# Kernel tuning notes

Hardware: AMD Instinct MI355X
Metric: run time of the kernel (lower is better)

The kernel has to match this reference:

```python
import jax, jax.numpy as jnp
import numpy as np

B, S, DIM, HDIM = 8, 1024, 1024, 128
H = DIM // HDIM  # 8 heads
GN_EPS = 1e-3    # keras GroupNormalization default epsilon


def group_norm(y, gamma, beta, groups, eps=GN_EPS):
    # keras GroupNormalization on [B,S,C]: reshape to [B,S,groups,C//groups],
    # normalize over all axes except batch and group axis -> axes (1,3).
    b, s, c = y.shape
    g = y.reshape(b, s, groups, c // groups)
    mean = g.mean(axis=(1, 3), keepdims=True)
    var = g.var(axis=(1, 3), keepdims=True)
    g = (g - mean) * jax.lax.rsqrt(var + eps)
    return g.reshape(b, s, c) * gamma + beta


def setup_inputs() -> dict:
    key = jax.random.key(0)
    ks = jax.random.split(key, 7)
    x = jax.random.normal(ks[0], (B, S, DIM), dtype=jnp.float32)
    sc_h = 1.0 / np.sqrt(HDIM).astype(np.float32)
    sc_d = 1.0 / np.sqrt(DIM).astype(np.float32)
    Wq = jax.random.normal(ks[1], (H, HDIM, HDIM), dtype=jnp.float32) * sc_h
    Wk = jax.random.normal(ks[2], (H, HDIM, HDIM), dtype=jnp.float32) * sc_h
    Wv = jax.random.normal(ks[3], (H, HDIM, HDIM), dtype=jnp.float32) * sc_h
    Wg = jax.random.normal(ks[4], (DIM, DIM), dtype=jnp.float32) * sc_d
    Wo = jax.random.normal(ks[5], (DIM, DIM), dtype=jnp.float32) * sc_d
    gn_gamma = jnp.ones((DIM,), dtype=jnp.float32)
    gn_beta = jnp.zeros((DIM,), dtype=jnp.float32)
    return {"x": x, "Wq": Wq, "Wk": Wk, "Wv": Wv, "Wg": Wg, "Wo": Wo,
            "gn_gamma": gn_gamma, "gn_beta": gn_beta}


def reference(x, Wq, Wk, Wv, Wg, Wo, gn_gamma, gn_beta):
    b, s, c = x.shape
    h, hd = Wq.shape[0], Wq.shape[1]
    # gating branch: W = ReLU(x @ Wg)
    Wgate = jax.nn.relu(jnp.einsum('bsc,cd->bsd', x, Wg))
    # split channels into heads: [B,S,H,hd]
    xh = x.reshape(b, s, h, hd)
    Q = jnp.einsum('bshd,hde->bhse', xh, Wq)
    K = jnp.einsum('bshd,hde->bhse', xh, Wk)
    V = jnp.einsum('bshd,hde->bhse', xh, Wv)
    # per-head decay mask D[h,i,j] = gamma_h ** (i - j) (full, non-causal as in source)
    idx = jnp.arange(s, dtype=jnp.float32)
    gammas = 1.0 - 2.0 ** (-5.0 - jnp.arange(h, dtype=jnp.float32))  # [H]
    decay = gammas[:, None, None] ** (idx[None, :, None] - idx[None, None, :])  # [H,S,S]
    scores = jnp.einsum('bhsd,bhtd->bhst', Q, K) * decay[None]
    ret = jnp.einsum('bhst,bhtd->bhsd', scores, V)       # [B,H,S,hd]
    y = ret.transpose(0, 2, 1, 3).reshape(b, s, c)        # concat heads
    Y = group_norm(y, gn_gamma, gn_beta, groups=hd)       # groups = hdim (keras arg)
    return jnp.einsum('bsc,cd->bsd', Wgate * Y, Wo)
```

## Files before the change

### kernel.cpp

```cpp
#include <hip/hip_runtime.h>

#define BB 8
#define SS 1024
#define DD 1024
#define HH 8
#define HD 128
#define GN_EPS 1e-3f

typedef __attribute__((ext_vector_type(8))) short bf16x8;
typedef __attribute__((ext_vector_type(4))) float f32x4;

__device__ __forceinline__ short f2bf(float f) {
    unsigned u = __float_as_uint(f);
    return (short)((u + 0x7fffu + ((u >> 16) & 1u)) >> 16);
}
__device__ __forceinline__ float bf2f(short s) {
    return __uint_as_float(((unsigned)(unsigned short)s) << 16);
}

__device__ __forceinline__ void gload16(const void* g, void* l) {
    __builtin_amdgcn_global_load_lds((const __attribute__((address_space(1))) void*)g,
                                     (__attribute__((address_space(3))) void*)l, 16, 0, 0);
}

__device__ __forceinline__ void stage_tile(const short* __restrict__ G, size_t ld, int k0,
                                           short* lds, int wid, int lane) {
#pragma unroll
    for (int i = 0; i < 2; i++) {
        const int seg = wid * 2 + i;
        const int row = seg * 8 + (lane >> 3);
        const int chunk = (lane & 7) ^ (lane >> 3);
        gload16(G + (size_t)row * ld + k0 + chunk * 8, lds + seg * 512);
    }
}

__device__ __forceinline__ void gemm_tile_g(
    const short* __restrict__ A, size_t ldA,
    const short* __restrict__ B, size_t ldB,
    int K, short* As, short* Bs, f32x4 acc[4][2])
{
    const int tid = threadIdx.x, lane = tid & 63, wid = tid >> 6;
    const int wr = (wid >> 2) * 64, wc = (wid & 3) * 32;
    const int fr = lane & 15, fc = lane >> 4;
    const int rsw = fr & 7;
#pragma unroll
    for (int i = 0; i < 4; i++)
#pragma unroll
        for (int j = 0; j < 2; j++) acc[i][j] = (f32x4){0.f, 0.f, 0.f, 0.f};

    const int nt = K >> 6;
    stage_tile(A, ldA, 0, As, wid, lane);
    stage_tile(B, ldB, 0, Bs, wid, lane);
    if (nt > 1) {
        stage_tile(A, ldA, 64, As + 8192, wid, lane);
        stage_tile(B, ldB, 64, Bs + 8192, wid, lane);
    }
    for (int t = 0; t < nt; t++) {
        if (t + 1 < nt) asm volatile("s_waitcnt vmcnt(4)" ::: "memory");
        else            asm volatile("s_waitcnt vmcnt(0)" ::: "memory");
        __builtin_amdgcn_s_barrier();
        __builtin_amdgcn_sched_barrier(0);
        const int cur = t & 1;
        const short* as = As + (cur << 13);
        const short* bs = Bs + (cur << 13);
#pragma unroll
        for (int half = 0; half < 2; half++) {
            const int slot = ((half * 4 + fc) ^ rsw) << 3;
            bf16x8 af[4], bfv[2];
#pragma unroll
            for (int i = 0; i < 4; i++) af[i] = *(const bf16x8*)&as[(wr + i * 16 + fr) * 64 + slot];
#pragma unroll
            for (int j = 0; j < 2; j++) bfv[j] = *(const bf16x8*)&bs[(wc + j * 16 + fr) * 64 + slot];
#pragma unroll
            for (int i = 0; i < 4; i++)
#pragma unroll
                for (int j = 0; j < 2; j++)
                    acc[i][j] = __builtin_amdgcn_mfma_f32_16x16x32_bf16(af[i], bfv[j], acc[i][j], 0, 0, 0);
        }
        __builtin_amdgcn_sched_barrier(0);
        asm volatile("s_waitcnt lgkmcnt(0)" ::: "memory");
        __builtin_amdgcn_s_barrier();
        if (t + 2 < nt) {
            stage_tile(A, ldA, (t + 2) << 6, As + (cur << 13), wid, lane);
            stage_tile(B, ldB, (t + 2) << 6, Bs + (cur << 13), wid, lane);
        }
    }
}

__device__ __forceinline__ void stage_A32(const short* __restrict__ G, size_t ld, int k0,
                                          short* lds, int wid, int lane) {
#pragma unroll
    for (int i = 0; i < 2; i++) {
        const int row = wid * 32 + i * 16 + (lane >> 2);
        const int chunk = (lane & 3) ^ ((row >> 1) & 3);
        gload16(G + (size_t)row * ld + k0 + chunk * 8, lds + wid * 1024 + i * 512);
    }
}
__device__ __forceinline__ void stage_B32(const short* __restrict__ G, size_t ld, int k0,
                                          short* lds, int wid, int lane) {
    const int row = wid * 16 + (lane >> 2);
    const int chunk = (lane & 3) ^ ((row >> 1) & 3);
    gload16(G + (size_t)row * ld + k0 + chunk * 8, lds + wid * 512);
}

__device__ __forceinline__ void gemm_tile_n(
    const short* __restrict__ A, size_t ldA,
    const short* __restrict__ B, size_t ldB,
    int K, short* As, short* Bs, f32x4 acc[4][4])
{
    const int tid = threadIdx.x, lane = tid & 63, wid = tid >> 6;
    const int wr = (wid >> 1) * 64, wc = (wid & 1) * 64;
    const int fr = lane & 15, fc = lane >> 4;
    const int slot = (fc ^ ((fr >> 1) & 3)) << 3;
#pragma unroll
    for (int i = 0; i < 4; i++)
#pragma unroll
        for (int j = 0; j < 4; j++) acc[i][j] = (f32x4){0.f, 0.f, 0.f, 0.f};

    const int nt = K >> 5;
    stage_A32(A, ldA, 0, As, wid, lane);
    stage_B32(B, ldB, 0, Bs, wid, lane);
    if (nt > 1) {
        stage_A32(A, ldA, 32, As + 8192, wid, lane);
        stage_B32(B, ldB, 32, Bs + 4096, wid, lane);
    }
    for (int t = 0; t < nt; t++) {
        if (t + 1 < nt) asm volatile("s_waitcnt vmcnt(3)" ::: "memory");
        else            asm volatile("s_waitcnt vmcnt(0)" ::: "memory");
        __builtin_amdgcn_s_barrier();
        __builtin_amdgcn_sched_barrier(0);
        const int cur = t & 1;
        const short* as = As + (cur << 13);
        const short* bs = Bs + (cur << 12);
        bf16x8 af[4], bfv[4];
#pragma unroll
        for (int i = 0; i < 4; i++) af[i] = *(const bf16x8*)&as[(wr + i * 16 + fr) * 32 + slot];
#pragma unroll
        for (int j = 0; j < 4; j++) bfv[j] = *(const bf16x8*)&bs[(wc + j * 16 + fr) * 32 + slot];
#pragma unroll
        for (int i = 0; i < 4; i++)
#pragma unroll
            for (int j = 0; j < 4; j++)
                acc[i][j] = __builtin_amdgcn_mfma_f32_16x16x32_bf16(af[i], bfv[j], acc[i][j], 0, 0, 0);
        __builtin_amdgcn_sched_barrier(0);
        asm volatile("s_waitcnt lgkmcnt(0)" ::: "memory");
        __builtin_amdgcn_s_barrier();
        if (t + 2 < nt) {
            stage_A32(A, ldA, (t + 2) << 5, As + (cur << 13), wid, lane);
            stage_B32(B, ldB, (t + 2) << 5, Bs + (cur << 12), wid, lane);
        }
    }
}

__global__ __launch_bounds__(256) void prep(
    const float* __restrict__ x,
    const float* __restrict__ Wq, const float* __restrict__ Wk, const float* __restrict__ Wv,
    const float* __restrict__ Wg, const float* __restrict__ Wo,
    short* __restrict__ xb, short* __restrict__ WgT, short* __restrict__ WoT,
    short* __restrict__ Wt, float* __restrict__ sQ, float* __restrict__ sK,
    float* __restrict__ Sp)
{
    __shared__ float t[32][33];
    int bid = blockIdx.x;
    const int tid = threadIdx.x;
    if (bid < 4096) {
        const size_t i = ((size_t)bid * 256 + tid) * 8;
        float4 a = *(const float4*)&x[i];
        float4 b = *(const float4*)&x[i + 4];
        bf16x8 v;
        v[0] = f2bf(a.x); v[1] = f2bf(a.y); v[2] = f2bf(a.z); v[3] = f2bf(a.w);
        v[4] = f2bf(b.x); v[5] = f2bf(b.y); v[6] = f2bf(b.z); v[7] = f2bf(b.w);
        *(bf16x8*)&xb[i] = v;
        return;
    }
    bid -= 4096;
    if (bid < 2048) {
        const float* __restrict__ S = (bid < 1024) ? Wg : Wo;
        short* __restrict__ D = (bid < 1024) ? WgT : WoT;
        const int tb = bid & 1023;
        const int bx = (tb & 31) * 32, by = (tb >> 5) * 32;
        const int xx = tid & 31, y0 = tid >> 5;
#pragma unroll
        for (int r = 0; r < 32; r += 8) t[y0 + r][xx] = S[(size_t)(by + y0 + r) * 1024 + bx + xx];
        __syncthreads();
#pragma unroll
        for (int r = 0; r < 32; r += 8) D[(size_t)(bx + y0 + r) * 1024 + by + xx] = f2bf(t[xx][y0 + r]);
        return;
    }
    bid -= 2048;
    if (bid < 384) {
        const int ht = bid >> 4, tb = bid & 15;
        const int typ = ht >> 3, h = ht & 7;
        const float* __restrict__ W = (typ == 0 ? Wq : (typ == 1 ? Wk : Wv)) + (size_t)h * HD * HD;
        short* __restrict__ D = Wt + (size_t)ht * HD * HD;
        const int bx = (tb & 3) * 32, by = (tb >> 2) * 32;
        const int xx = tid & 31, y0 = tid >> 5;
#pragma unroll
        for (int r = 0; r < 32; r += 8) t[y0 + r][xx] = W[(by + y0 + r) * HD + bx + xx];
        __syncthreads();
#pragma unroll
        for (int r = 0; r < 32; r += 8) D[(bx + y0 + r) * HD + by + xx] = f2bf(t[xx][y0 + r]);
        return;
    }
    bid -= 384;
    if (bid < 32) {
        const int h = bid >> 2;
        const int s = (bid & 3) * 256 + tid;
        const double gamma = 1.0 - exp2((double)(-5 - h));
        const double lg = log2(gamma);
        sQ[h * SS + s] = (float)exp2(lg * (double)s);
        sK[h * SS + s] = (float)exp2(-lg * (double)s);
        return;
    }
    *(float4*)&Sp[tid * 8] = (float4){0.f, 0.f, 0.f, 0.f};
    *(float4*)&Sp[tid * 8 + 4] = (float4){0.f, 0.f, 0.f, 0.f};
}

__global__ __launch_bounds__(512) void g_qkvgate(
    const short* __restrict__ xb, const short* __restrict__ Wt, const short* __restrict__ WgT,
    const float* __restrict__ sQ, const float* __restrict__ sK,
    short* __restrict__ Qb, short* __restrict__ Ktb, short* __restrict__ Vtb,
    short* __restrict__ gateb)
{
    __shared__ short As[2 * 8192], Bs[2 * 8192];
    const int orig = blockIdx.x;
    const int cx = orig & 7, p = orig >> 3;
    const int tid = threadIdx.x, lane = tid & 63, wid = tid >> 6;
    const int r0 = (lane >> 4) * 4, c = lane & 15;

    if (p < 32) {
        f32x4 acc[4][4];
        const int w2 = cx * 32 + p;
        const int m0 = (w2 >> 3) * 256, n0 = (w2 & 7) * 128;
        gemm_tile_n(xb + (size_t)m0 * DD, DD, WgT + (size_t)n0 * DD, DD, DD, As, Bs, acc);
        const int wr = (wid >> 1) * 64, wc = (wid & 1) * 64;
#pragma unroll
        for (int i = 0; i < 4; i++)
#pragma unroll
            for (int j = 0; j < 4; j++)
#pragma unroll
                for (int r = 0; r < 4; r++)
                    gateb[(size_t)(m0 + wr + i * 16 + r0 + r) * DD + n0 + wc + j * 16 + c] =
                        f2bf(fmaxf(acc[i][j][r], 0.f));
        return;
    }
    f32x4 acc[4][2];
    const int w = cx * 64 + (p - 32);
    const int mt = w >> 3, h = w & 7;
    const int m0 = mt * 128;
    const int b = m0 >> 10, s0 = m0 & (SS - 1);
    const int bh = (b << 3) + h;
    const short* __restrict__ A = xb + (size_t)m0 * DD + h * HD;
    const int wr = (wid >> 2) * 64, wc = (wid & 3) * 32;
    const int fr = lane & 15, fc = lane >> 4;
    const int rsw = fr & 7;

    stage_tile(A, DD, 0,  As,        wid, lane);
    stage_tile(A, DD, 64, As + 8192, wid, lane);
    stage_tile(Wt + (size_t)h * HD * HD, HD, 0, Bs, wid, lane);
    __syncthreads();

#pragma unroll
    for (int i = 0; i < 4; i++)
#pragma unroll
        for (int j = 0; j < 2; j++) acc[i][j] = (f32x4){0.f, 0.f, 0.f, 0.f};

    int sb = 0;
    for (int st = 0; st < 6; st++) {
        if (st + 1 < 6) {
            const int typn = (st + 1) >> 1, ktn = (st + 1) & 1;
            stage_tile(Wt + (size_t)(typn * 8 + h) * HD * HD, HD, ktn * 64,
                       Bs + ((sb ^ 1) << 13), wid, lane);
        }
        const int kt = st & 1;
        const short* as = As + (kt << 13);
        const short* bs = Bs + (sb << 13);
#pragma unroll
        for (int half = 0; half < 2; half++) {
            const int slot = ((half * 4 + fc) ^ rsw) << 3;
            bf16x8 af[4], bfv[2];
#pragma unroll
            for (int i = 0; i < 4; i++) af[i] = *(const bf16x8*)&as[(wr + i * 16 + fr) * 64 + slot];
#pragma unroll
            for (int j = 0; j < 2; j++) bfv[j] = *(const bf16x8*)&bs[(wc + j * 16 + fr) * 64 + slot];
#pragma unroll
            for (int i = 0; i < 4; i++)
#pragma unroll
                for (int j = 0; j < 2; j++)
                    acc[i][j] = __builtin_amdgcn_mfma_f32_16x16x32_bf16(af[i], bfv[j], acc[i][j], 0, 0, 0);
        }
        __syncthreads();
        sb ^= 1;
        if (kt == 1) {
            const int typ = st >> 1;
            if (typ == 0) {
#pragma unroll
                for (int i = 0; i < 4; i++)
#pragma unroll
                    for (int j = 0; j < 2; j++)
#pragma unroll
                        for (int r = 0; r < 4; r++) {
                            const int s = s0 + wr + i * 16 + r0 + r;
                            Qb[((size_t)bh * SS + s) * HD + wc + j * 16 + c] =
                                f2bf(acc[i][j][r] * sQ[h * SS + s]);
                        }
            } else if (typ == 1) {
                short* __restrict__ Ob = Ktb + (size_t)bh * HD * SS;
#pragma unroll
                for (int i = 0; i < 4; i++)
#pragma unroll
                    for (int j = 0; j < 2; j++) {
                        const int tb = s0 + wr + i * 16 + r0;
                        const int d = wc + j * 16 + c;
                        short4 o;
                        o.x = f2bf(acc[i][j][0] * sK[h * SS + tb + 0]);
                        o.y = f2bf(acc[i][j][1] * sK[h * SS + tb + 1]);
                        o.z = f2bf(acc[i][j][2] * sK[h * SS + tb + 2]);
                        o.w = f2bf(acc[i][j][3] * sK[h * SS + tb + 3]);
                        *(short4*)&Ob[(size_t)d * SS + tb] = o;
                    }
            } else {
                short* __restrict__ Ob = Vtb + (size_t)bh * HD * SS;
#pragma unroll
                for (int i = 0; i < 4; i++)
#pragma unroll
                    for (int j = 0; j < 2; j++) {
                        const int tb = s0 + wr + i * 16 + r0;
                        const int e = wc + j * 16 + c;
                        short4 o;
                        o.x = f2bf(acc[i][j][0]); o.y = f2bf(acc[i][j][1]);
                        o.z = f2bf(acc[i][j][2]); o.w = f2bf(acc[i][j][3]);
                        *(short4*)&Ob[(size_t)e * SS + tb] = o;
                    }
            }
#pragma unroll
            for (int i = 0; i < 4; i++)
#pragma unroll
                for (int j = 0; j < 2; j++) acc[i][j] = (f32x4){0.f, 0.f, 0.f, 0.f};
        }
    }
}

__global__ __launch_bounds__(512) void g_kv(
    const short* __restrict__ Vtb, const short* __restrict__ Ktb, float* __restrict__ Mp)
{
    __shared__ short As[2 * 8192], Bs[2 * 8192];
    f32x4 acc[4][2];
    const int orig = blockIdx.x;
    const int w = (orig & 7) * 16 + (orig >> 3);
    const int chunk = w & 1, bh = w >> 1;
    gemm_tile_g(Vtb + (size_t)bh * HD * SS + chunk * 512, SS,
                Ktb + (size_t)bh * HD * SS + chunk * 512, SS, 512, As, Bs, acc);
    const int tid = threadIdx.x, lane = tid & 63, wid = tid >> 6;
    const int wr = (wid >> 2) * 64, wc = (wid & 3) * 32;
    const int r0 = (lane >> 4) * 4, c = lane & 15;
    float* __restrict__ Ob = Mp + (size_t)w * HD * HD;
#pragma unroll
    for (int i = 0; i < 4; i++)
#pragma unroll
        for (int j = 0; j < 2; j++)
#pragma unroll
            for (int r = 0; r < 4; r++)
                Ob[(size_t)(wr + i * 16 + r0 + r) * HD + wc + j * 16 + c] = acc[i][j][r];
}

__global__ __launch_bounds__(256) void g_mredcvt(const float* __restrict__ Mp, short* __restrict__ Mtb) {
    const size_t i = ((size_t)blockIdx.x * 256 + threadIdx.x) * 8;
    const size_t bh = i >> 14, ij = i & 16383;
    const float* p = Mp + (bh * 2) * 16384 + ij;
    float s[8];
#pragma unroll
    for (int q = 0; q < 8; q++) s[q] = 0.f;
#pragma unroll
    for (int cth = 0; cth < 2; cth++) {
        float4 a = *(const float4*)&p[cth * 16384];
        float4 b = *(const float4*)&p[cth * 16384 + 4];
        s[0] += a.x; s[1] += a.y; s[2] += a.z; s[3] += a.w;
        s[4] += b.x; s[5] += b.y; s[6] += b.z; s[7] += b.w;
    }
    bf16x8 v;
#pragma unroll
    for (int q = 0; q < 8; q++) v[q] = f2bf(s[q]);
    *(bf16x8*)&Mtb[i] = v;
}

__global__ __launch_bounds__(512) void g_qm(
    const short* __restrict__ Qb, const short* __restrict__ Mtb,
    short* __restrict__ retc, float* __restrict__ Sp)
{
    __shared__ short As[2 * 8192], Bs[2 * 8192];
    f32x4 acc[4][2];
    const int orig = blockIdx.x;
    const int w = (orig & 7) * 64 + (orig >> 3);
    const int bh = w >> 3, m0 = (w & 7) * 128;
    const short* __restrict__ A = Qb + ((size_t)bh * SS + m0) * HD;
    const short* __restrict__ Bp = Mtb + (size_t)bh * HD * HD;
    const int tid = threadIdx.x, lane = tid & 63, wid = tid >> 6;
    const int wr = (wid >> 2) * 64, wc = (wid & 3) * 32;
    const int fr = lane & 15, fc = lane >> 4, rsw = fr & 7;
    const int r0 = (lane >> 4) * 4, c = lane & 15;

    stage_tile(A,  HD, 0,  As,        wid, lane);
    stage_tile(A,  HD, 64, As + 8192, wid, lane);
    stage_tile(Bp, HD, 0,  Bs,        wid, lane);
    stage_tile(Bp, HD, 64, Bs + 8192, wid, lane);
#pragma unroll
    for (int i = 0; i < 4; i++)
#pragma unroll
        for (int j = 0; j < 2; j++) acc[i][j] = (f32x4){0.f, 0.f, 0.f, 0.f};
    asm volatile("s_waitcnt vmcnt(0)" ::: "memory");
    __builtin_amdgcn_s_barrier();
    __builtin_amdgcn_sched_barrier(0);
#pragma unroll
    for (int kt = 0; kt < 2; kt++) {
        const short* as = As + (kt << 13);
        const short* bs = Bs + (kt << 13);
#pragma unroll
        for (int half = 0; half < 2; half++) {
            const int slot = ((half * 4 + fc) ^ rsw) << 3;
            bf16x8 af[4], bfv[2];
#pragma unroll
            for (int i = 0; i < 4; i++) af[i] = *(const bf16x8*)&as[(wr + i * 16 + fr) * 64 + slot];
#pragma unroll
            for (int j = 0; j < 2; j++) bfv[j] = *(const bf16x8*)&bs[(wc + j * 16 + fr) * 64 + slot];
#pragma unroll
            for (int i = 0; i < 4; i++)
#pragma unroll
                for (int j = 0; j < 2; j++)
                    acc[i][j] = __builtin_amdgcn_mfma_f32_16x16x32_bf16(af[i], bfv[j], acc[i][j], 0, 0, 0);
        }
    }
    const int b_ = bh >> 3, h_ = bh & 7;
    short* __restrict__ O = retc + ((size_t)(b_ * SS + m0)) * DD + h_ * HD;
#pragma unroll
    for (int i = 0; i < 4; i++)
#pragma unroll
        for (int j = 0; j < 2; j++)
#pragma unroll
            for (int r = 0; r < 4; r++)
                O[(size_t)(wr + i * 16 + r0 + r) * DD + wc + j * 16 + c] = f2bf(acc[i][j][r]);

    float psm[2], psq[2];
#pragma unroll
    for (int j = 0; j < 2; j++) { psm[j] = 0.f; psq[j] = 0.f; }
#pragma unroll
    for (int i = 0; i < 4; i++)
#pragma unroll
        for (int j = 0; j < 2; j++)
#pragma unroll
            for (int r = 0; r < 4; r++) {
                const float v = acc[i][j][r];
                psm[j] += v; psq[j] += v * v;
            }
    const int masks[5] = {1, 2, 4, 16, 32};
#pragma unroll
    for (int mk = 0; mk < 5; mk++) {
#pragma unroll
        for (int j = 0; j < 2; j++) {
            psm[j] += __shfl_xor(psm[j], masks[mk], 64);
            psq[j] += __shfl_xor(psq[j], masks[mk], 64);
        }
    }
    if ((lane & 7) == 0 && lane < 16) {
        const int hi = lane >> 3;
#pragma unroll
        for (int j = 0; j < 2; j++) {
            const int g = b_ * 128 + h_ * 16 + (wid & 3) * 4 + j * 2 + hi;
            atomicAdd(&Sp[g * 2 + 0], psm[j]);
            atomicAdd(&Sp[g * 2 + 1], psq[j]);
        }
    }
}

__global__ __launch_bounds__(256) void aprep(
    const short* __restrict__ gateb, const short* __restrict__ retc,
    const float* __restrict__ Sp,
    const float* __restrict__ gng, const float* __restrict__ gnb, short* __restrict__ Ab)
{
    const size_t idx = ((size_t)blockIdx.x * 256 + threadIdx.x) * 4;
    const int m = (int)(idx >> 10), cc = (int)(idx & 1023);
    const int b_ = m >> 10, g = b_ * 128 + (cc >> 3);
    const float sm = Sp[g * 2 + 0], sq = Sp[g * 2 + 1];
    const float mu = sm * (1.0f / 8192.0f);
    float var = sq * (1.0f / 8192.0f) - mu * mu;
    if (var < 0.f) var = 0.f;
    const float rs = rsqrtf(var + GN_EPS);
    short4 gv4 = *(const short4*)&gateb[idx];
    short4 rv4 = *(const short4*)&retc[idx];
    float4 gv = *(const float4*)&gng[cc];
    float4 bv = *(const float4*)&gnb[cc];
    short4 o;
    o.x = f2bf(bf2f(gv4.x) * ((bf2f(rv4.x) - mu) * rs * gv.x + bv.x));
    o.y = f2bf(bf2f(gv4.y) * ((bf2f(rv4.y) - mu) * rs * gv.y + bv.y));
    o.z = f2bf(bf2f(gv4.z) * ((bf2f(rv4.z) - mu) * rs * gv.z + bv.z));
    o.w = f2bf(bf2f(gv4.w) * ((bf2f(rv4.w) - mu) * rs * gv.w + bv.w));
    *(short4*)&Ab[idx] = o;
}

__global__ __launch_bounds__(512) void g_final(
    const short* __restrict__ Ab, const short* __restrict__ WoT, float* __restrict__ out)
{
    __shared__ short As[2 * 8192], Bs[2 * 4096];
    f32x4 acc[4][4];
    const int orig = blockIdx.x;
    const int w = (orig & 7) * 32 + (orig >> 3);
    const int m0 = (w >> 3) * 256, n0 = (w & 7) * 128;
    gemm_tile_n(Ab + (size_t)m0 * DD, DD, WoT + (size_t)n0 * DD, DD, DD, As, Bs, acc);
    const int tid = threadIdx.x, lane = tid & 63, wid = tid >> 6;
    const int wr = (wid >> 1) * 64, wc = (wid & 1) * 64;
    const int r0 = (lane >> 4) * 4, c = lane & 15;
#pragma unroll
    for (int i = 0; i < 4; i++)
#pragma unroll
        for (int j = 0; j < 4; j++)
#pragma unroll
            for (int r = 0; r < 4; r++)
                out[(size_t)(m0 + wr + i * 16 + r0 + r) * DD + n0 + wc + j * 16 + c] = acc[i][j][r];
}

extern "C" void kernel_launch(void* const* d_in, const int* in_sizes, int n_in,
                              void* d_out, int out_size, void* d_ws, size_t ws_size,
                              hipStream_t stream)
{
    const float* x   = (const float*)d_in[0];
    const float* Wq  = (const float*)d_in[1];
    const float* Wk  = (const float*)d_in[2];
    const float* Wv  = (const float*)d_in[3];
    const float* Wg  = (const float*)d_in[4];
    const float* Wo  = (const float*)d_in[5];
    const float* gng = (const float*)d_in[6];
    const float* gnb = (const float*)d_in[7];
    float* out = (float*)d_out;

    char* ws = (char*)d_ws;
    size_t off = 0;
    auto alloc = [&](size_t bytes) -> void* {
        void* p = ws + off;
        off += (bytes + 255) & ~(size_t)255;
        return p;
    };
    const size_t NE = (size_t)BB * SS * DD;
    float*  sQ    = (float*)alloc((size_t)HH * SS * sizeof(float));
    float*  sK    = (float*)alloc((size_t)HH * SS * sizeof(float));
    short*  xb    = (short*)alloc(NE * sizeof(short));
    short*  WgT   = (short*)alloc((size_t)DD * DD * sizeof(short));
    short*  WoT   = (short*)alloc((size_t)DD * DD * sizeof(short));
    short*  Wt    = (short*)alloc((size_t)24 * HD * HD * sizeof(short));
    short*  Qb    = (short*)alloc(NE * sizeof(short));
    short*  Ktb   = (short*)alloc(NE * sizeof(short));
    short*  Vtb   = (short*)alloc(NE * sizeof(short));
    short*  retc  = (short*)alloc(NE * sizeof(short));
    short*  gateb = (short*)alloc(NE * sizeof(short));
    short*  Ab    = (short*)alloc(NE * sizeof(short));
    float*  Mp    = (float*)alloc((size_t)128 * HD * HD * sizeof(float));
    short*  Mtb   = (short*)alloc((size_t)64 * HD * HD * sizeof(short));
    float*  Sp    = (float*)alloc((size_t)1024 * 2 * sizeof(float));

    prep<<<dim3(6561), 256, 0, stream>>>(x, Wq, Wk, Wv, Wg, Wo, xb, WgT, WoT, Wt, sQ, sK, Sp);
    g_qkvgate<<<dim3(768), 512, 0, stream>>>(xb, Wt, WgT, sQ, sK, Qb, Ktb, Vtb, gateb);
    g_kv<<<dim3(128), 512, 0, stream>>>(Vtb, Ktb, Mp);
    g_mredcvt<<<dim3(512), 256, 0, stream>>>(Mp, Mtb);
    g_qm<<<dim3(512), 512, 0, stream>>>(Qb, Mtb, retc, Sp);
    aprep<<<dim3(8192), 256, 0, stream>>>(gateb, retc, Sp, gng, gnb, Ab);
    g_final<<<dim3(256), 512, 0, stream>>>(Ab, WoT, out);
}
```

Before: 117.4 us.

## Triple-buffer GEMM LDS staging and async-pipeline the QKV projection loads

The shared GEMM tile loop now rotates through three LDS stages instead of two, and raises wave priority around the MFMA block with s_setprio. The per-head Q/K/V projection path drops __syncthreads in favour of explicit vmcnt waits and barriers, prefetching weight tiles two steps ahead into a double-buffered B region. The aim is to overlap global-to-LDS loads with MFMA work and cut barrier stalls. In exchange, LDS use per block grows to 72KB, which may limit occupancy, and the post-compute barrier is still kept.

Measured after the change: 113.7 us. 3.2% less time.

```diff
diff --git a/kernel.cpp b/kernel.cpp
--- a/kernel.cpp
+++ b/kernel.cpp
@@ -103,7 +103,7 @@
     gload16(G + (size_t)row * ld + k0 + chunk * 8, lds + wid * 512);
 }
 
-__device__ __forceinline__ void gemm_tile_n(
+__device__ __forceinline__ void gemm_tile_3(
     const short* __restrict__ A, size_t ldA,
     const short* __restrict__ B, size_t ldB,
     int K, short* As, short* Bs, f32x4 acc[4][4])
@@ -124,31 +124,35 @@
         stage_A32(A, ldA, 32, As + 8192, wid, lane);
         stage_B32(B, ldB, 32, Bs + 4096, wid, lane);
     }
+    int cur = 0;
     for (int t = 0; t < nt; t++) {
         if (t + 1 < nt) asm volatile("s_waitcnt vmcnt(3)" ::: "memory");
         else            asm volatile("s_waitcnt vmcnt(0)" ::: "memory");
         __builtin_amdgcn_s_barrier();
         __builtin_amdgcn_sched_barrier(0);
-        const int cur = t & 1;
-        const short* as = As + (cur << 13);
-        const short* bs = Bs + (cur << 12);
+        const short* as = As + cur * 8192;
+        const short* bs = Bs + cur * 4096;
         bf16x8 af[4], bfv[4];
 #pragma unroll
         for (int i = 0; i < 4; i++) af[i] = *(const bf16x8*)&as[(wr + i * 16 + fr) * 32 + slot];
 #pragma unroll
         for (int j = 0; j < 4; j++) bfv[j] = *(const bf16x8*)&bs[(wc + j * 16 + fr) * 32 + slot];
+        __builtin_amdgcn_s_setprio(1);
 #pragma unroll
         for (int i = 0; i < 4; i++)
 #pragma unroll
             for (int j = 0; j < 4; j++)
                 acc[i][j] = __builtin_amdgcn_mfma_f32_16x16x32_bf16(af[i], bfv[j], acc[i][j], 0, 0, 0);
+        __builtin_amdgcn_s_setprio(0);
         __builtin_amdgcn_sched_barrier(0);
         asm volatile("s_waitcnt lgkmcnt(0)" ::: "memory");
         __builtin_amdgcn_s_barrier();
         if (t + 2 < nt) {
-            stage_A32(A, ldA, (t + 2) << 5, As + (cur << 13), wid, lane);
-            stage_B32(B, ldB, (t + 2) << 5, Bs + (cur << 12), wid, lane);
-        }
+            int nb = cur + 2; if (nb >= 3) nb -= 3;
+            stage_A32(A, ldA, (t + 2) << 5, As + nb * 8192, wid, lane);
+            stage_B32(B, ldB, (t + 2) << 5, Bs + nb * 4096, wid, lane);
+        }
+        cur = (cur + 1 == 3) ? 0 : cur + 1;
     }
 }
 
@@ -222,7 +226,7 @@
     short* __restrict__ Qb, short* __restrict__ Ktb, short* __restrict__ Vtb,
     short* __restrict__ gateb)
 {
-    __shared__ short As[2 * 8192], Bs[2 * 8192];
+    __shared__ short lds[36864];
     const int orig = blockIdx.x;
     const int cx = orig & 7, p = orig >> 3;
     const int tid = threadIdx.x, lane = tid & 63, wid = tid >> 6;
@@ -232,7 +236,8 @@
         f32x4 acc[4][4];
         const int w2 = cx * 32 + p;
         const int m0 = (w2 >> 3) * 256, n0 = (w2 & 7) * 128;
-        gemm_tile_n(xb + (size_t)m0 * DD, DD, WgT + (size_t)n0 * DD, DD, DD, As, Bs, acc);
+        gemm_tile_3(xb + (size_t)m0 * DD, DD, WgT + (size_t)n0 * DD, DD, DD,
+                    lds, lds + 24576, acc);
         const int wr = (wid >> 1) * 64, wc = (wid & 1) * 64;
 #pragma unroll
         for (int i = 0; i < 4; i++)
@@ -245,6 +250,8 @@
         return;
     }
     f32x4 acc[4][2];
+    short* As = lds;
+    short* Bs = lds + 16384;
     const int w = cx * 64 + (p - 32);
     const int mt = w >> 3, h = w & 7;
     const int m0 = mt * 128;
@@ -257,24 +264,22 @@
 
     stage_tile(A, DD, 0,  As,        wid, lane);
     stage_tile(A, DD, 64, As + 8192, wid, lane);
-    stage_tile(Wt + (size_t)h * HD * HD, HD, 0, Bs, wid, lane);
-    __syncthreads();
+    stage_tile(Wt + (size_t)h * HD * HD, HD, 0,  Bs,        wid, lane);
+    stage_tile(Wt + (size_t)h * HD * HD, HD, 64, Bs + 8192, wid, lane);
 
 #pragma unroll
     for (int i = 0; i < 4; i++)
 #pragma unroll
         for (int j = 0; j < 2; j++) acc[i][j] = (f32x4){0.f, 0.f, 0.f, 0.f};
 
-    int sb = 0;
     for (int st = 0; st < 6; st++) {
-        if (st + 1 < 6) {
-            const int typn = (st + 1) >> 1, ktn = (st + 1) & 1;
-            stage_tile(Wt + (size_t)(typn * 8 + h) * HD * HD, HD, ktn * 64,
-                       Bs + ((sb ^ 1) << 13), wid, lane);
-        }
+        if (st + 1 < 6) asm volatile("s_waitcnt vmcnt(2)" ::: "memory");
+        else            asm volatile("s_waitcnt vmcnt(0)" ::: "memory");
+        __builtin_amdgcn_s_barrier();
+        __builtin_amdgcn_sched_barrier(0);
         const int kt = st & 1;
         const short* as = As + (kt << 13);
-        const short* bs = Bs + (sb << 13);
+        const short* bs = Bs + (kt << 13);
 #pragma unroll
         for (int half = 0; half < 2; half++) {
             const int slot = ((half * 4 + fc) ^ rsw) << 3;
@@ -289,8 +294,9 @@
                 for (int j = 0; j < 2; j++)
                     acc[i][j] = __builtin_amdgcn_mfma_f32_16x16x32_bf16(af[i], bfv[j], acc[i][j], 0, 0, 0);
         }
-        __syncthreads();
-        sb ^= 1;
+        __builtin_amdgcn_sched_barrier(0);
+        asm volatile("s_waitcnt lgkmcnt(0)" ::: "memory");
+        __builtin_amdgcn_s_barrier();
         if (kt == 1) {
             const int typ = st >> 1;
             if (typ == 0) {
@@ -337,6 +343,12 @@
             for (int i = 0; i < 4; i++)
 #pragma unroll
                 for (int j = 0; j < 2; j++) acc[i][j] = (f32x4){0.f, 0.f, 0.f, 0.f};
+        }
+        __builtin_amdgcn_sched_barrier(0);
+        if (st + 2 < 6) {
+            const int typn = (st + 2) >> 1, ktn = (st + 2) & 1;
+            stage_tile(Wt + (size_t)(typn * 8 + h) * HD * HD, HD, ktn * 64,
+                       Bs + (kt << 13), wid, lane);
         }
     }
 }
@@ -500,12 +512,13 @@
 __global__ __launch_bounds__(512) void g_final(
     const short* __restrict__ Ab, const short* __restrict__ WoT, float* __restrict__ out)
 {
-    __shared__ short As[2 * 8192], Bs[2 * 4096];
+    __shared__ short lds[36864];
     f32x4 acc[4][4];
     const int orig = blockIdx.x;
     const int w = (orig & 7) * 32 + (orig >> 3);
     const int m0 = (w >> 3) * 256, n0 = (w & 7) * 128;
-    gemm_tile_n(Ab + (size_t)m0 * DD, DD, WoT + (size_t)n0 * DD, DD, DD, As, Bs, acc);
+    gemm_tile_3(Ab + (size_t)m0 * DD, DD, WoT + (size_t)n0 * DD, DD, DD,
+                lds, lds + 24576, acc);
     const int tid = threadIdx.x, lane = tid & 63, wid = tid >> 6;
     const int wr = (wid >> 1) * 64, wc = (wid & 1) * 64;
     const int r0 = (lane >> 4) * 4, c = lane & 15;
```
